# Performance work log

Hardware: AMD Instinct MI355X
Metric: run time of the kernel (lower is better)

Reference implementation:

```python
import jax, jax.numpy as jnp
import numpy as np

NH = 8      # num_heads
NP_ = 4     # num_points

def setup_inputs() -> dict:
    key = jax.random.key(0)
    ks = jax.random.split(key, 12)
    B, N, C = 8, 4096, 256
    query = jax.random.normal(ks[0], (B, N, C), jnp.float32)
    value = jax.random.normal(ks[1], (B, N, C), jnp.float32)
    reference_points = jax.random.uniform(ks[2], (B, N, 2), jnp.float32)
    xav = lambda k, i, o: jax.random.normal(k, (i, o), jnp.float32) * np.sqrt(2.0 / (i + o)).astype(np.float32)
    W_off = jax.random.normal(ks[3], (C, NH * NP_ * 2), jnp.float32) * 0.02  # small offsets (orig inits to 0)
    b_off = jax.random.normal(ks[4], (NH * NP_ * 2,), jnp.float32) * 0.02
    W_attn = xav(ks[5], C, NH * NP_)
    b_attn = jnp.zeros((NH * NP_,), jnp.float32)
    W_val = xav(ks[6], C, C)
    b_val = jnp.zeros((C,), jnp.float32)
    W_out = xav(ks[7], C, C)
    b_out = jnp.zeros((C,), jnp.float32)
    return dict(query=query, value=value, reference_points=reference_points,
                W_off=W_off, b_off=b_off, W_attn=W_attn, b_attn=b_attn,
                W_val=W_val, b_val=b_val, W_out=W_out, b_out=b_out)

def _deform_attn(query, value, reference_points, W_off, b_off, W_attn, b_attn, W_val, b_val, W_out, b_out):
    B, N, C = query.shape
    HW = value.shape[1]
    H = W = int(np.sqrt(HW))  # static
    hd = C // NH
    # value projection -> [B, NH, H*W, hd]
    vals = (value @ W_val + b_val).reshape(B, H, W, NH, hd)
    vals = vals.transpose(0, 3, 1, 2, 4).reshape(B, NH, H * W, hd)
    # offsets [B,N,NH,P,2] in [-0.5,0.5]; attention weights softmax over P
    off = jnp.tanh((query @ W_off + b_off).reshape(B, N, NH, NP_, 2)) * 0.5
    attn = jax.nn.softmax((query @ W_attn + b_attn).reshape(B, N, NH, NP_), axis=-1)
    # sampling locations in [0,1], then grid coords in [-1,1] (x=width, y=height)
    loc = jnp.clip(reference_points[:, :, None, None, :] + off, 0.0, 1.0)
    g = loc * 2.0 - 1.0
    # torch grid_sample, align_corners=False: pixel = (g+1)*size/2 - 0.5
    x = (g[..., 0] + 1.0) * (W * 0.5) - 0.5
    y = (g[..., 1] + 1.0) * (H * 0.5) - 0.5
    x0f = jnp.floor(x); y0f = jnp.floor(y)
    wx1 = x - x0f; wx0 = 1.0 - wx1
    wy1 = y - y0f; wy0 = 1.0 - wy1
    x0 = x0f.astype(jnp.int32); x1 = x0 + 1
    y0 = y0f.astype(jnp.int32); y1 = y0 + 1

    def corner(xi, yi, w):  # xi,yi,w: [B,N,NH,P]; zero padding outside
        valid = (xi >= 0) & (xi < W) & (yi >= 0) & (yi < H)
        idx = jnp.clip(yi, 0, H - 1) * W + jnp.clip(xi, 0, W - 1)
        idx_h = idx.transpose(0, 2, 1, 3).reshape(B, NH, N * NP_)      # [B,NH,N*P]
        gat = jnp.take_along_axis(vals, idx_h[..., None], axis=2)      # [B,NH,N*P,hd]
        wv = jnp.where(valid, w, 0.0).transpose(0, 2, 1, 3).reshape(B, NH, N * NP_)
        return gat * wv[..., None]

    sampled = (corner(x0, y0, wx0 * wy0) + corner(x1, y0, wx1 * wy0)
               + corner(x0, y1, wx0 * wy1) + corner(x1, y1, wx1 * wy1))
    sampled = sampled.reshape(B, NH, N, NP_, hd)
    attn_h = attn.transpose(0, 2, 1, 3)                                 # [B,NH,N,P]
    out = jnp.einsum('bhnpd,bhnp->bnhd', sampled, attn_h).reshape(B, N, C)
    return out @ W_out + b_out  # dropout is identity in eval

def reference(query, value, reference_points, W_off, b_off, W_attn, b_attn, W_val, b_val, W_out, b_out):
    return _deform_attn(query, value, reference_points, W_off, b_off, W_attn, b_attn, W_val, b_val, W_out, b_out)
```

## Files before the change

kernel.cpp:

```cpp
#include <hip/hip_runtime.h>
#include <math.h>

#define NHEAD 8
#define NPT 4
#define HDIM 32
#define IMG 64
#define CDIM 256
#define NQ 4096
#define BATCH 8
#define MTOT (BATCH * NQ)

typedef __attribute__((ext_vector_type(8))) short bf16x8;
typedef __attribute__((ext_vector_type(4))) float f32x4;

__device__ __forceinline__ unsigned short f2b(float f) {
    union { float f; unsigned u; } v; v.f = f;
    unsigned r = (v.u + 0x7FFFu + ((v.u >> 16) & 1u)) >> 16;
    return (unsigned short)r;
}
__device__ __forceinline__ float b2f(unsigned short u) {
    union { unsigned u; float f; } v; v.u = ((unsigned)u) << 16;
    return v.f;
}

#define SWZ(row, col)   ((col) ^ (((row) & 7) << 3))
#define SWZ32(row, col) ((col) ^ (((row) & 3) << 3))

__device__ __forceinline__ void gload16(const void* src, void* ldsbase) {
    __builtin_amdgcn_global_load_lds(
        (const __attribute__((address_space(1))) void*)src,
        (__attribute__((address_space(3))) void*)ldsbase, 16, 0, 0);
}


__global__ __launch_bounds__(256)
void cvt_weights_kernel(const float* __restrict__ Wv, const float* __restrict__ Wo,
                        const float* __restrict__ Woff, const float* __restrict__ Wattn,
                        const float* __restrict__ boff, const float* __restrict__ battn,
                        unsigned short* __restrict__ Wv_t, unsigned short* __restrict__ Wo_t,
                        unsigned short* __restrict__ Wl_h, unsigned short* __restrict__ Wl_l,
                        float* __restrict__ bias_lin)
{
    int tid = blockIdx.x * 256 + threadIdx.x;
    int n = tid & 255, k = tid >> 8;
    Wv_t[n * 256 + k] = f2b(Wv[k * 256 + n]);
    Wo_t[n * 256 + k] = f2b(Wo[k * 256 + n]);
    if (tid < 128 * 256) {
        int nn = tid >> 8;
        int kk = tid & 255;
        float v = (nn < 64) ? Woff[kk * 64 + nn]
                : (nn < 96) ? Wattn[kk * 32 + (nn - 64)] : 0.f;
        unsigned short hi = f2b(v);
        unsigned short lo = f2b(v - b2f(hi));
        Wl_h[nn * 256 + kk] = hi;
        Wl_l[nn * 256 + kk] = lo;
    }
    if (tid < 128)
        bias_lin[tid] = (tid < 64) ? boff[tid] : (tid < 96) ? battn[tid - 64] : 0.f;
}

__global__ __launch_bounds__(256)
void fused_gemms_kernel(const float* __restrict__ value,
                        const float* __restrict__ query,
                        const unsigned short* __restrict__ Wv_t,
                        const unsigned short* __restrict__ Wl_h,
                        const unsigned short* __restrict__ Wl_l,
                        const float* __restrict__ b_val,
                        const float* __restrict__ bias_lin,
                        unsigned short* __restrict__ projv,
                        float* __restrict__ lin)
{
    __shared__ char smem[32768];

    const int tid  = threadIdx.x;
    const int lane = tid & 63;
    const int wid  = tid >> 6;
    const int wr = (wid >> 1) * 64;
    const int wc = (wid & 1) * 64;
    const int l15 = lane & 15;
    const int lk  = (lane >> 4) * 8;

    f32x4 acc[4][4];
    #pragma unroll
    for (int m = 0; m < 4; ++m)
        #pragma unroll
        for (int n = 0; n < 4; ++n)
            #pragma unroll
            for (int r = 0; r < 4; ++r) acc[m][n][r] = 0.f;

    if (blockIdx.x < 512) {
        unsigned short (*As)[64] = (unsigned short(*)[64])smem;
        unsigned short (*Bs)[64] = (unsigned short(*)[64])(smem + 16384);
        const int bx = blockIdx.x;
        const int gm = ((bx & 7) << 12) + (((bx >> 3) & 31) << 7);
        const int gn = (bx >> 8) << 7;
        const int rl  = lane >> 3;
        const int ch  = (lane & 7) ^ (rl & 7);

        for (int k0 = 0; k0 < 256; k0 += 64) {
            #pragma unroll
            for (int it = 0; it < 4; ++it) {
                const int br = it * 32 + wid * 8;
                gload16(&Wv_t[(size_t)(gn + br + rl) * 256 + k0 + ch * 8], &Bs[br][0]);
            }
            #pragma unroll
            for (int it = 0; it < 4; ++it) {
                const int chunk = it * 256 + tid;
                const int row = chunk >> 3;
                const int kc  = (chunk & 7) << 3;
                const float4* src = (const float4*)&value[(size_t)(gm + row) * 256 + k0 + kc];
                const float4 a = src[0], b = src[1];
                float f[8] = {a.x, a.y, a.z, a.w, b.x, b.y, b.z, b.w};
                unsigned short h[8];
                #pragma unroll
                for (int j = 0; j < 8; ++j) h[j] = f2b(f[j]);
                *(uint4*)&As[row][SWZ(row, kc)] = *(const uint4*)h;
            }
            __syncthreads();

            #pragma unroll
            for (int kk = 0; kk < 64; kk += 32) {
                bf16x8 a[4], b[4];
                #pragma unroll
                for (int m = 0; m < 4; ++m) {
                    const int r = wr + m * 16 + l15;
                    a[m] = *(const bf16x8*)&As[r][SWZ(r, kk + lk)];
                }
                #pragma unroll
                for (int n = 0; n < 4; ++n) {
                    const int r = wc + n * 16 + l15;
                    b[n] = *(const bf16x8*)&Bs[r][SWZ(r, kk + lk)];
                }
                #pragma unroll
                for (int m = 0; m < 4; ++m)
                    #pragma unroll
                    for (int n = 0; n < 4; ++n)
                        acc[m][n] = __builtin_amdgcn_mfma_f32_16x16x32_bf16(a[m], b[n], acc[m][n], 0, 0, 0);
            }
            __syncthreads();
        }

        const int cr = (lane >> 4) * 4;
        #pragma unroll
        for (int n = 0; n < 4; ++n) {
            const int col = gn + wc + n * 16 + l15;
            const float bv = b_val[col];
            #pragma unroll
            for (int m = 0; m < 4; ++m)
                #pragma unroll
                for (int r = 0; r < 4; ++r) {
                    const int row = gm + wr + m * 16 + cr + r;
                    projv[(size_t)row * 256 + col] = f2b(acc[m][n][r] + bv);
                }
        }
    } else {
        unsigned short (*Ah)[32] = (unsigned short(*)[32])smem;
        unsigned short (*Al)[32] = (unsigned short(*)[32])(smem + 8192);
        unsigned short (*Bh)[32] = (unsigned short(*)[32])(smem + 16384);
        unsigned short (*Bl)[32] = (unsigned short(*)[32])(smem + 24576);
        const int lbx = blockIdx.x - 512;
        const int gm = ((lbx & 7) << 12) + ((lbx >> 3) << 7);
        const int rs = lane >> 2;
        const int cc = lane & 3;

        for (int k0 = 0; k0 < 256; k0 += 32) {
            #pragma unroll
            for (int i = 0; i < 2; ++i) {
                const int row = wid * 32 + i * 16 + rs;
                const int cs = (cc ^ (row & 3)) << 3;
                gload16(&Wl_h[(size_t)row * 256 + k0 + cs], &Bh[wid * 32 + i * 16][0]);
                gload16(&Wl_l[(size_t)row * 256 + k0 + cs], &Bl[wid * 32 + i * 16][0]);
            }
            #pragma unroll
            for (int it = 0; it < 2; ++it) {
                const int chunk = it * 256 + tid;
                const int row = chunk >> 2;
                const int kc  = (chunk & 3) << 3;
                const float4* src = (const float4*)&query[(size_t)(gm + row) * 256 + k0 + kc];
                const float4 a = src[0], b = src[1];
                float f[8] = {a.x, a.y, a.z, a.w, b.x, b.y, b.z, b.w};
                unsigned short h[8], l[8];
                #pragma unroll
                for (int j = 0; j < 8; ++j) {
                    h[j] = f2b(f[j]);
                    l[j] = f2b(f[j] - b2f(h[j]));
                }
                const int sc = SWZ32(row, kc);
                *(uint4*)&Ah[row][sc] = *(const uint4*)h;
                *(uint4*)&Al[row][sc] = *(const uint4*)l;
            }
            __syncthreads();

            bf16x8 ah[4], al[4];
            #pragma unroll
            for (int m = 0; m < 4; ++m) {
                const int r = wr + m * 16 + l15;
                const int c = SWZ32(r, lk);
                ah[m] = *(const bf16x8*)&Ah[r][c];
                al[m] = *(const bf16x8*)&Al[r][c];
            }
            if (wc == 0) {
                bf16x8 bh[4], bl[4];
                #pragma unroll
                for (int n = 0; n < 4; ++n) {
                    const int r = n * 16 + l15;
                    const int c = SWZ32(r, lk);
                    bh[n] = *(const bf16x8*)&Bh[r][c];
                    bl[n] = *(const bf16x8*)&Bl[r][c];
                }
                #pragma unroll
                for (int m = 0; m < 4; ++m)
                    #pragma unroll
                    for (int n = 0; n < 4; ++n) {
                        acc[m][n] = __builtin_amdgcn_mfma_f32_16x16x32_bf16(ah[m], bh[n], acc[m][n], 0, 0, 0);
                        acc[m][n] = __builtin_amdgcn_mfma_f32_16x16x32_bf16(ah[m], bl[n], acc[m][n], 0, 0, 0);
                        acc[m][n] = __builtin_amdgcn_mfma_f32_16x16x32_bf16(al[m], bh[n], acc[m][n], 0, 0, 0);
                    }
            } else {
                bf16x8 bh[2], bl[2];
                #pragma unroll
                for (int n = 0; n < 2; ++n) {
                    const int r = 64 + n * 16 + l15;
                    const int c = SWZ32(r, lk);
                    bh[n] = *(const bf16x8*)&Bh[r][c];
                    bl[n] = *(const bf16x8*)&Bl[r][c];
                }
                #pragma unroll
                for (int m = 0; m < 4; ++m)
                    #pragma unroll
                    for (int n = 0; n < 2; ++n) {
                        acc[m][n] = __builtin_amdgcn_mfma_f32_16x16x32_bf16(ah[m], bh[n], acc[m][n], 0, 0, 0);
                        acc[m][n] = __builtin_amdgcn_mfma_f32_16x16x32_bf16(ah[m], bl[n], acc[m][n], 0, 0, 0);
                        acc[m][n] = __builtin_amdgcn_mfma_f32_16x16x32_bf16(al[m], bh[n], acc[m][n], 0, 0, 0);
                    }
            }
            __syncthreads();
        }

        const int cr = (lane >> 4) * 4;
        #pragma unroll
        for (int n = 0; n < 4; ++n) {
            const int col = wc + n * 16 + l15;
            if (col < 96) {
                const float bv = bias_lin[col];
                #pragma unroll
                for (int m = 0; m < 4; ++m)
                    #pragma unroll
                    for (int r = 0; r < 4; ++r) {
                        const int row = gm + wr + m * 16 + cr + r;
                        lin[(size_t)row * 96 + col] = acc[m][n][r] + bv;
                    }
            }
        }
    }
}

__global__ __launch_bounds__(256)
void gemm_out_kernel(const unsigned short* __restrict__ Ap,
                     const unsigned short* __restrict__ Bt,
                     const float* __restrict__ bias,
                     float* __restrict__ C)
{
    __shared__ unsigned short As[128][64];
    __shared__ unsigned short Bs[128][64];

    const int tid  = threadIdx.x;
    const int lane = tid & 63;
    const int wid  = tid >> 6;
    const int gm = ((blockIdx.x & 7) << 12) + ((blockIdx.x >> 3) << 7);
    const int gn = blockIdx.y * 128;
    const int wr = (wid >> 1) * 64;
    const int wc = (wid & 1) * 64;
    const int l15 = lane & 15;
    const int lk  = (lane >> 4) * 8;
    const int rl  = lane >> 3;
    const int ch  = (lane & 7) ^ (rl & 7);

    f32x4 acc[4][4];
    #pragma unroll
    for (int m = 0; m < 4; ++m)
        #pragma unroll
        for (int n = 0; n < 4; ++n)
            #pragma unroll
            for (int r = 0; r < 4; ++r) acc[m][n][r] = 0.f;

    for (int k0 = 0; k0 < 256; k0 += 64) {
        #pragma unroll
        for (int it = 0; it < 4; ++it) {
            const int br = it * 32 + wid * 8;
            gload16(&Bt[(size_t)(gn + br + rl) * 256 + k0 + ch * 8], &Bs[br][0]);
            gload16(&Ap[(size_t)(gm + br + rl) * 256 + k0 + ch * 8], &As[br][0]);
        }
        __syncthreads();

        #pragma unroll
        for (int kk = 0; kk < 64; kk += 32) {
            bf16x8 a[4], b[4];
            #pragma unroll
            for (int m = 0; m < 4; ++m) {
                const int r = wr + m * 16 + l15;
                a[m] = *(const bf16x8*)&As[r][SWZ(r, kk + lk)];
            }
            #pragma unroll
            for (int n = 0; n < 4; ++n) {
                const int r = wc + n * 16 + l15;
                b[n] = *(const bf16x8*)&Bs[r][SWZ(r, kk + lk)];
            }
            #pragma unroll
            for (int m = 0; m < 4; ++m)
                #pragma unroll
                for (int n = 0; n < 4; ++n)
                    acc[m][n] = __builtin_amdgcn_mfma_f32_16x16x32_bf16(a[m], b[n], acc[m][n], 0, 0, 0);
        }
        __syncthreads();
    }

    const int cr = (lane >> 4) * 4;
    #pragma unroll
    for (int n = 0; n < 4; ++n) {
        const int col = gn + wc + n * 16 + l15;
        const float bv = bias[col];
        #pragma unroll
        for (int m = 0; m < 4; ++m)
            #pragma unroll
            for (int r = 0; r < 4; ++r) {
                const int row = gm + wr + m * 16 + cr + r;
                C[(size_t)row * 256 + col] = acc[m][n][r] + bv;
            }
    }
}

__global__ __launch_bounds__(256)
void sample_gather_kernel(const unsigned short* __restrict__ projv,
                          const float* __restrict__ lin,
                          const float* __restrict__ refp,
                          unsigned short* __restrict__ sampled)
{
    __shared__ float4 s_w[8][32];
    __shared__ unsigned s_xy[8][32];

    const int i = blockIdx.x;
    const int b = i & 7;
    const int bn0 = (b << 12) + ((i >> 3) << 3);
    const int t = threadIdx.x;

    {
        const int sub = t >> 5;
        const int q = t & 31;
        const int h = q >> 2;
        const int p = q & 3;
        const int bn = bn0 + sub;
        const float2 rp = *(const float2*)&refp[(size_t)bn * 2];
        const float2 ol = *(const float2*)&lin[(size_t)bn * 96 + h * 8 + p * 2];
        const float al  = lin[(size_t)bn * 96 + 64 + q];

        float mx = al;
        mx = fmaxf(mx, __shfl_xor(mx, 1));
        mx = fmaxf(mx, __shfl_xor(mx, 2));
        float e = expf(al - mx);
        float s = e;
        s += __shfl_xor(s, 1);
        s += __shfl_xor(s, 2);
        const float aw = e / s;

        const float lx = fminf(fmaxf(rp.x + tanhf(ol.x) * 0.5f, 0.f), 1.f);
        const float ly = fminf(fmaxf(rp.y + tanhf(ol.y) * 0.5f, 0.f), 1.f);
        const float x = lx * (float)IMG - 0.5f;
        const float y = ly * (float)IMG - 0.5f;
        const float x0f = floorf(x), y0f = floorf(y);
        const int x0 = (int)x0f, y0 = (int)y0f;
        const float wx1 = x - x0f, wx0 = 1.f - wx1;
        const float wy1 = y - y0f, wy0 = 1.f - wy1;
        const bool vx0 = (x0 >= 0), vx1 = (x0 + 1 < IMG);
        const bool vy0 = (y0 >= 0), vy1 = (y0 + 1 < IMG);
        float4 w;
        w.x = (vx0 && vy0) ? wx0 * wy0 * aw : 0.f;
        w.y = (vx1 && vy0) ? wx1 * wy0 * aw : 0.f;
        w.z = (vx0 && vy1) ? wx0 * wy1 * aw : 0.f;
        w.w = (vx1 && vy1) ? wx1 * wy1 * aw : 0.f;
        const int x0c = min(max(x0, 0), IMG - 1), x1c = min(max(x0 + 1, 0), IMG - 1);
        const int y0c = min(max(y0, 0), IMG - 1), y1c = min(max(y0 + 1, 0), IMG - 1);
        s_w[sub][q] = w;
        s_xy[sub][q] = (unsigned)x0c | ((unsigned)x1c << 8) | ((unsigned)y0c << 16) | ((unsigned)y1c << 24);
    }
    __syncthreads();

    const int l = t & 63;
    const int h2 = l >> 3;
    const int cp = l & 7;
    const unsigned short* vbase = projv + ((size_t)b << 20) + h2 * HDIM + cp * 4;

    #pragma unroll
    for (int pass = 0; pass < 2; ++pass) {
        const int sub = (t >> 6) + pass * 4;
        const int bn = bn0 + sub;

        float a0 = 0.f, a1 = 0.f, a2 = 0.f, a3 = 0.f;
        #pragma unroll
        for (int p = 0; p < 4; ++p) {
            const float4 w = s_w[sub][h2 * 4 + p];
            const unsigned xy = s_xy[sub][h2 * 4 + p];
            const int x0 = xy & 255, x1 = (xy >> 8) & 255;
            const int y0 = (xy >> 16) & 255, y1 = xy >> 24;
            const uint2 u00 = *(const uint2*)&vbase[(((y0 << 6) + x0) << 8)];
            const uint2 u01 = *(const uint2*)&vbase[(((y0 << 6) + x1) << 8)];
            const uint2 u10 = *(const uint2*)&vbase[(((y1 << 6) + x0) << 8)];
            const uint2 u11 = *(const uint2*)&vbase[(((y1 << 6) + x1) << 8)];
            a0 += w.x * b2f((unsigned short)(u00.x & 0xffff)) + w.y * b2f((unsigned short)(u01.x & 0xffff))
                + w.z * b2f((unsigned short)(u10.x & 0xffff)) + w.w * b2f((unsigned short)(u11.x & 0xffff));
            a1 += w.x * b2f((unsigned short)(u00.x >> 16)) + w.y * b2f((unsigned short)(u01.x >> 16))
                + w.z * b2f((unsigned short)(u10.x >> 16)) + w.w * b2f((unsigned short)(u11.x >> 16));
            a2 += w.x * b2f((unsigned short)(u00.y & 0xffff)) + w.y * b2f((unsigned short)(u01.y & 0xffff))
                + w.z * b2f((unsigned short)(u10.y & 0xffff)) + w.w * b2f((unsigned short)(u11.y & 0xffff));
            a3 += w.x * b2f((unsigned short)(u00.y >> 16)) + w.y * b2f((unsigned short)(u01.y >> 16))
                + w.z * b2f((unsigned short)(u10.y >> 16)) + w.w * b2f((unsigned short)(u11.y >> 16));
        }
        uint2 outp;
        outp.x = (unsigned)f2b(a0) | ((unsigned)f2b(a1) << 16);
        outp.y = (unsigned)f2b(a2) | ((unsigned)f2b(a3) << 16);
        *(uint2*)&sampled[(size_t)bn * 256 + h2 * HDIM + cp * 4] = outp;
    }
}

extern "C" void kernel_launch(void* const* d_in, const int* in_sizes, int n_in,
                              void* d_out, int out_size, void* d_ws, size_t ws_size,
                              hipStream_t stream)
{
    const float* query  = (const float*)d_in[0];
    const float* value  = (const float*)d_in[1];
    const float* refp   = (const float*)d_in[2];
    const float* W_off  = (const float*)d_in[3];
    const float* b_off  = (const float*)d_in[4];
    const float* W_attn = (const float*)d_in[5];
    const float* b_attn = (const float*)d_in[6];
    const float* W_val  = (const float*)d_in[7];
    const float* b_val  = (const float*)d_in[8];
    const float* W_out  = (const float*)d_in[9];
    const float* b_out  = (const float*)d_in[10];
    float* out = (float*)d_out;

    char* ws = (char*)d_ws;
    unsigned short* projv    = (unsigned short*)ws; ws += (size_t)MTOT * 256 * 2;
    unsigned short* sampled  = (unsigned short*)ws; ws += (size_t)MTOT * 256 * 2;
    float*          lin      = (float*)ws;          ws += (size_t)MTOT * 96 * 4;
    unsigned short* Wv_t     = (unsigned short*)ws; ws += 256 * 256 * 2;
    unsigned short* Wo_t     = (unsigned short*)ws; ws += 256 * 256 * 2;
    unsigned short* Wl_h     = (unsigned short*)ws; ws += 128 * 256 * 2;
    unsigned short* Wl_l     = (unsigned short*)ws; ws += 128 * 256 * 2;
    float*          bias_lin = (float*)ws;          ws += 128 * 4;

    dim3 blk(256);

    cvt_weights_kernel<<<dim3(256), blk, 0, stream>>>(W_val, W_out, W_off, W_attn, b_off, b_attn,
                                                      Wv_t, Wo_t, Wl_h, Wl_l, bias_lin);

    fused_gemms_kernel<<<dim3(768), blk, 0, stream>>>(value, query, Wv_t, Wl_h, Wl_l,
                                                      b_val, bias_lin, projv, lin);

    sample_gather_kernel<<<dim3(MTOT / 8), blk, 0, stream>>>(projv, lin, refp, sampled);

    gemm_out_kernel<<<dim3(MTOT / 128, 2), blk, 0, stream>>>(sampled, Wo_t, b_out, out);
}
```

Before: 73.28 us.

## Pre-convert value to bf16 and use direct-to-LDS loads in fused GEMMs

Adds a separate kernel that converts the fp32 value tensor to bf16 in workspace, so the value-projection GEMM can stage A tiles with global_load_lds instead of register loads plus conversion. The query GEMM now loads fp32 query directly into LDS and splits it into hi/lo bf16 in registers at fragment-read time. Block ordering is swapped so the query blocks come first. The cost is an extra full read and write pass over value (about 16 MB of traffic) plus one more kernel launch.

```diff
diff --git a/kernel.cpp b/kernel.cpp
--- a/kernel.cpp
+++ b/kernel.cpp
@@ -24,7 +24,6 @@
 }
 
 #define SWZ(row, col)   ((col) ^ (((row) & 7) << 3))
-#define SWZ32(row, col) ((col) ^ (((row) & 3) << 3))
 
 __device__ __forceinline__ void gload16(const void* src, void* ldsbase) {
     __builtin_amdgcn_global_load_lds(
@@ -32,6 +31,19 @@
         (__attribute__((address_space(3))) void*)ldsbase, 16, 0, 0);
 }
 
+
+__global__ __launch_bounds__(256)
+void cvt_value_kernel(const float* __restrict__ in, unsigned short* __restrict__ out)
+{
+    const int n8 = MTOT * 256 / 8;
+    for (int i = blockIdx.x * 256 + threadIdx.x; i < n8; i += 2048 * 256) {
+        const float4 a = ((const float4*)in)[i * 2];
+        const float4 b = ((const float4*)in)[i * 2 + 1];
+        unsigned short us[8] = { f2b(a.x), f2b(a.y), f2b(a.z), f2b(a.w),
+                                 f2b(b.x), f2b(b.y), f2b(b.z), f2b(b.w) };
+        ((uint4*)out)[i] = *(const uint4*)us;
+    }
+}
 
 __global__ __launch_bounds__(256)
 void cvt_weights_kernel(const float* __restrict__ Wv, const float* __restrict__ Wo,
@@ -60,7 +72,7 @@
 }
 
 __global__ __launch_bounds__(256)
-void fused_gemms_kernel(const float* __restrict__ value,
+void fused_gemms_kernel(const unsigned short* __restrict__ value_bf,
                         const float* __restrict__ query,
                         const unsigned short* __restrict__ Wv_t,
                         const unsigned short* __restrict__ Wl_h,
@@ -88,33 +100,21 @@
             #pragma unroll
             for (int r = 0; r < 4; ++r) acc[m][n][r] = 0.f;
 
-    if (blockIdx.x < 512) {
+    if (blockIdx.x >= 256) {
         unsigned short (*As)[64] = (unsigned short(*)[64])smem;
         unsigned short (*Bs)[64] = (unsigned short(*)[64])(smem + 16384);
-        const int bx = blockIdx.x;
+        const int bx = blockIdx.x - 256;
         const int gm = ((bx & 7) << 12) + (((bx >> 3) & 31) << 7);
         const int gn = (bx >> 8) << 7;
         const int rl  = lane >> 3;
-        const int ch  = (lane & 7) ^ (rl & 7);
+        const int ch  = (lane & 7) ^ rl;
 
         for (int k0 = 0; k0 < 256; k0 += 64) {
             #pragma unroll
             for (int it = 0; it < 4; ++it) {
                 const int br = it * 32 + wid * 8;
                 gload16(&Wv_t[(size_t)(gn + br + rl) * 256 + k0 + ch * 8], &Bs[br][0]);
-            }
-            #pragma unroll
-            for (int it = 0; it < 4; ++it) {
-                const int chunk = it * 256 + tid;
-                const int row = chunk >> 3;
-                const int kc  = (chunk & 7) << 3;
-                const float4* src = (const float4*)&value[(size_t)(gm + row) * 256 + k0 + kc];
-                const float4 a = src[0], b = src[1];
-                float f[8] = {a.x, a.y, a.z, a.w, b.x, b.y, b.z, b.w};
-                unsigned short h[8];
-                #pragma unroll
-                for (int j = 0; j < 8; ++j) h[j] = f2b(f[j]);
-                *(uint4*)&As[row][SWZ(row, kc)] = *(const uint4*)h;
+                gload16(&value_bf[(size_t)(gm + br + rl) * 256 + k0 + ch * 8], &As[br][0]);
             }
             __syncthreads();
 
@@ -154,85 +154,63 @@
                 }
         }
     } else {
-        unsigned short (*Ah)[32] = (unsigned short(*)[32])smem;
-        unsigned short (*Al)[32] = (unsigned short(*)[32])(smem + 8192);
+        float (*Aq)[32] = (float(*)[32])smem;
         unsigned short (*Bh)[32] = (unsigned short(*)[32])(smem + 16384);
         unsigned short (*Bl)[32] = (unsigned short(*)[32])(smem + 24576);
-        const int lbx = blockIdx.x - 512;
+        const int lbx = blockIdx.x;
         const int gm = ((lbx & 7) << 12) + ((lbx >> 3) << 7);
-        const int rs = lane >> 2;
-        const int cc = lane & 3;
+        const int rla = lane >> 3;
+        const int ca  = (lane & 7) ^ rla;
+        const int rsb = lane >> 2;
+        const int cb  = (lane & 3) ^ (rsb & 3);
 
         for (int k0 = 0; k0 < 256; k0 += 32) {
             #pragma unroll
+            for (int i = 0; i < 4; ++i) {
+                const int ar = wid * 32 + i * 8;
+                gload16(&query[(size_t)(gm + ar + rla) * 256 + k0 + ca * 4], &Aq[ar][0]);
+            }
+            #pragma unroll
             for (int i = 0; i < 2; ++i) {
-                const int row = wid * 32 + i * 16 + rs;
-                const int cs = (cc ^ (row & 3)) << 3;
-                gload16(&Wl_h[(size_t)row * 256 + k0 + cs], &Bh[wid * 32 + i * 16][0]);
-                gload16(&Wl_l[(size_t)row * 256 + k0 + cs], &Bl[wid * 32 + i * 16][0]);
-            }
-            #pragma unroll
-            for (int it = 0; it < 2; ++it) {
-                const int chunk = it * 256 + tid;
-                const int row = chunk >> 2;
-                const int kc  = (chunk & 3) << 3;
-                const float4* src = (const float4*)&query[(size_t)(gm + row) * 256 + k0 + kc];
-                const float4 a = src[0], b = src[1];
-                float f[8] = {a.x, a.y, a.z, a.w, b.x, b.y, b.z, b.w};
+                const int br = wid * 32 + i * 16;
+                gload16(&Wl_h[(size_t)(br + rsb) * 256 + k0 + cb * 8], &Bh[br][0]);
+                gload16(&Wl_l[(size_t)(br + rsb) * 256 + k0 + cb * 8], &Bl[br][0]);
+            }
+            __syncthreads();
+
+            bf16x8 ah[4], al[4];
+            #pragma unroll
+            for (int m = 0; m < 4; ++m) {
+                const int r = wr + m * 16 + l15;
+                const int c0 = ((lk >> 2) ^ (r & 7)) << 2;
+                const int c1 = (((lk >> 2) + 1) ^ (r & 7)) << 2;
+                const f32x4 qa = *(const f32x4*)&Aq[r][c0];
+                const f32x4 qb = *(const f32x4*)&Aq[r][c1];
+                float f[8] = {qa.x, qa.y, qa.z, qa.w, qb.x, qb.y, qb.z, qb.w};
                 unsigned short h[8], l[8];
                 #pragma unroll
                 for (int j = 0; j < 8; ++j) {
                     h[j] = f2b(f[j]);
                     l[j] = f2b(f[j] - b2f(h[j]));
                 }
-                const int sc = SWZ32(row, kc);
-                *(uint4*)&Ah[row][sc] = *(const uint4*)h;
-                *(uint4*)&Al[row][sc] = *(const uint4*)l;
-            }
-            __syncthreads();
-
-            bf16x8 ah[4], al[4];
-            #pragma unroll
-            for (int m = 0; m < 4; ++m) {
-                const int r = wr + m * 16 + l15;
-                const int c = SWZ32(r, lk);
-                ah[m] = *(const bf16x8*)&Ah[r][c];
-                al[m] = *(const bf16x8*)&Al[r][c];
-            }
-            if (wc == 0) {
-                bf16x8 bh[4], bl[4];
-                #pragma unroll
-                for (int n = 0; n < 4; ++n) {
-                    const int r = n * 16 + l15;
-                    const int c = SWZ32(r, lk);
-                    bh[n] = *(const bf16x8*)&Bh[r][c];
-                    bl[n] = *(const bf16x8*)&Bl[r][c];
+                ah[m] = *(const bf16x8*)h;
+                al[m] = *(const bf16x8*)l;
+            }
+
+            const int nN = (wc == 0) ? 4 : 2;
+            #pragma unroll
+            for (int n = 0; n < 4; ++n) {
+                if (n >= nN) break;
+                const int r = wc + n * 16 + l15;
+                const int c = ((lk >> 3) ^ (r & 3)) << 3;
+                const bf16x8 bh = *(const bf16x8*)&Bh[r][c];
+                const bf16x8 bl = *(const bf16x8*)&Bl[r][c];
+                #pragma unroll
+                for (int m = 0; m < 4; ++m) {
+                    acc[m][n] = __builtin_amdgcn_mfma_f32_16x16x32_bf16(ah[m], bh, acc[m][n], 0, 0, 0);
+                    acc[m][n] = __builtin_amdgcn_mfma_f32_16x16x32_bf16(ah[m], bl, acc[m][n], 0, 0, 0);
+                    acc[m][n] = __builtin_amdgcn_mfma_f32_16x16x32_bf16(al[m], bh, acc[m][n], 0, 0, 0);
                 }
-                #pragma unroll
-                for (int m = 0; m < 4; ++m)
-                    #pragma unroll
-                    for (int n = 0; n < 4; ++n) {
-                        acc[m][n] = __builtin_amdgcn_mfma_f32_16x16x32_bf16(ah[m], bh[n], acc[m][n], 0, 0, 0);
-                        acc[m][n] = __builtin_amdgcn_mfma_f32_16x16x32_bf16(ah[m], bl[n], acc[m][n], 0, 0, 0);
-                        acc[m][n] = __builtin_amdgcn_mfma_f32_16x16x32_bf16(al[m], bh[n], acc[m][n], 0, 0, 0);
-                    }
-            } else {
-                bf16x8 bh[2], bl[2];
-                #pragma unroll
-                for (int n = 0; n < 2; ++n) {
-                    const int r = 64 + n * 16 + l15;
-                    const int c = SWZ32(r, lk);
-                    bh[n] = *(const bf16x8*)&Bh[r][c];
-                    bl[n] = *(const bf16x8*)&Bl[r][c];
-                }
-                #pragma unroll
-                for (int m = 0; m < 4; ++m)
-                    #pragma unroll
-                    for (int n = 0; n < 2; ++n) {
-                        acc[m][n] = __builtin_amdgcn_mfma_f32_16x16x32_bf16(ah[m], bh[n], acc[m][n], 0, 0, 0);
-                        acc[m][n] = __builtin_amdgcn_mfma_f32_16x16x32_bf16(ah[m], bl[n], acc[m][n], 0, 0, 0);
-                        acc[m][n] = __builtin_amdgcn_mfma_f32_16x16x32_bf16(al[m], bh[n], acc[m][n], 0, 0, 0);
-                    }
             }
             __syncthreads();
         }
@@ -274,7 +252,7 @@
     const int l15 = lane & 15;
     const int lk  = (lane >> 4) * 8;
     const int rl  = lane >> 3;
-    const int ch  = (lane & 7) ^ (rl & 7);
+    const int ch  = (lane & 7) ^ rl;
 
     f32x4 acc[4][4];
     #pragma unroll
@@ -442,6 +420,7 @@
     char* ws = (char*)d_ws;
     unsigned short* projv    = (unsigned short*)ws; ws += (size_t)MTOT * 256 * 2;
     unsigned short* sampled  = (unsigned short*)ws; ws += (size_t)MTOT * 256 * 2;
+    unsigned short* value_bf = (unsigned short*)ws; ws += (size_t)MTOT * 256 * 2;
     float*          lin      = (float*)ws;          ws += (size_t)MTOT * 96 * 4;
     unsigned short* Wv_t     = (unsigned short*)ws; ws += 256 * 256 * 2;
     unsigned short* Wo_t     = (unsigned short*)ws; ws += 256 * 256 * 2;
@@ -453,8 +432,9 @@
 
     cvt_weights_kernel<<<dim3(256), blk, 0, stream>>>(W_val, W_out, W_off, W_attn, b_off, b_attn,
                                                       Wv_t, Wo_t, Wl_h, Wl_l, bias_lin);
-
-    fused_gemms_kernel<<<dim3(768), blk, 0, stream>>>(value, query, Wv_t, Wl_h, Wl_l,
+    cvt_value_kernel<<<dim3(2048), blk, 0, stream>>>(value, value_bf);
+
+    fused_gemms_kernel<<<dim3(768), blk, 0, stream>>>(value_bf, query, Wv_t, Wl_h, Wl_l,
                                                       b_val, bias_lin, projv, lin);
 
     sample_gather_kernel<<<dim3(MTOT / 8), blk, 0, stream>>>(projv, lin, refp, sampled);
```

New measurement: 72.07 us. No clear change (-1.7%).
